# Kernel tuning notes

Measured on AMD Instinct MI355X. Metric: run time of the kernel, lower is better.

Reference implementation:

```python
import jax, jax.numpy as jnp
import numpy as np

N = 4096        # n_locations
D_MODEL = 512
H, D_K, D_V = 4, 128, 256


def setup_inputs() -> dict:
    key = jax.random.key(0)
    ks = jax.random.split(key, 7)
    s = 0.02
    return {
        "Q": jax.random.normal(ks[0], (N, D_MODEL), dtype=jnp.float32),
        "K": jax.random.normal(ks[1], (N, D_MODEL), dtype=jnp.float32),
        "V": jax.random.normal(ks[2], (N, D_MODEL), dtype=jnp.float32),
        "Wq": jax.random.normal(ks[3], (H, D_MODEL, D_K), dtype=jnp.float32) * s,
        "Wk": jax.random.normal(ks[4], (H, D_MODEL, D_K), dtype=jnp.float32) * s,
        "Wv": jax.random.normal(ks[5], (H, D_MODEL, D_V), dtype=jnp.float32) * s,
        "Wo": jax.random.normal(ks[6], (D_MODEL, H * D_V), dtype=jnp.float32) * s,
    }


def reference(Q, K, V, Wq, Wk, Wv, Wo):
    n = K.shape[0]
    # Batched per-head projections: [h, n, d_k] / [h, n, d_v]
    q = jnp.einsum('nd,hdk->hnk', Q, Wq)
    k = jnp.einsum('nd,hdk->hnk', K, Wk)
    v = jnp.einsum('nd,hdv->hnv', V, Wv)
    # NOTE: original scales by sqrt(n_locations) (K.size(0)), not sqrt(d_k)
    scores = jnp.einsum('hqk,hnk->hqn', q, k) / jnp.sqrt(jnp.asarray(n, q.dtype))
    weights = jax.nn.softmax(scores, axis=-1)          # [h, n, n]
    heads = jnp.einsum('hqn,hnv->hqv', weights, v)      # [h, n, d_v]
    # concat heads along feature dim: [n, h*d_v]
    x = jnp.transpose(heads, (1, 0, 2)).reshape(heads.shape[1], -1)
    return x @ Wo.T                                     # [n, d_model]
```

## Files before the change

### kernel.cpp

```cpp
#include <hip/hip_runtime.h>
#include <hip/hip_bf16.h>
#include <type_traits>

typedef __hip_bfloat16 bf16;
typedef __attribute__((ext_vector_type(8))) short bf16x8;
typedef __attribute__((ext_vector_type(4))) float f32x4;

#define N_LOC 4096

__device__ __forceinline__ bf16 to_bf16(float f) { return __float2bfloat16(f); }

__device__ __forceinline__ void dma16(const bf16* g, bf16* l) {
  __builtin_amdgcn_global_load_lds((const __attribute__((address_space(1))) unsigned int*)g,
                                   (__attribute__((address_space(3))) unsigned int*)l, 16, 0, 0);
}

__global__ __launch_bounds__(256) void prep(const float* __restrict__ Q, const float* __restrict__ K,
                                            const float* __restrict__ V, const float* __restrict__ Wo,
                                            bf16* __restrict__ Qb, bf16* __restrict__ Kb,
                                            bf16* __restrict__ Vb, bf16* __restrict__ Wob,
                                            const float* __restrict__ Wq, const float* __restrict__ Wk,
                                            const float* __restrict__ Wv,
                                            bf16* __restrict__ oq, bf16* __restrict__ ok,
                                            bf16* __restrict__ ov) {
  __shared__ float tile[64][65];
  if (blockIdx.x < 3328) {
    long i = ((long)blockIdx.x * 256 + threadIdx.x) * 8;
    const float* src;
    bf16* dst;
    long off;
    if (i < 2097152)      { src = Q;  dst = Qb;  off = i; }
    else if (i < 4194304) { src = K;  dst = Kb;  off = i - 2097152; }
    else if (i < 6291456) { src = V;  dst = Vb;  off = i - 4194304; }
    else                  { src = Wo; dst = Wob; off = i - 6291456; }
    float4 a = *(const float4*)&src[off];
    float4 b = *(const float4*)&src[off + 4];
    union { bf16 h[8]; bf16x8 v; } u;
    u.h[0] = to_bf16(a.x); u.h[1] = to_bf16(a.y); u.h[2] = to_bf16(a.z); u.h[3] = to_bf16(a.w);
    u.h[4] = to_bf16(b.x); u.h[5] = to_bf16(b.y); u.h[6] = to_bf16(b.z); u.h[7] = to_bf16(b.w);
    *(bf16x8*)&dst[off] = u.v;
  } else {
    int pid = blockIdx.x - 3328;
    int z = pid >> 7;
    int rem = pid & 127;
    int xx = rem & 7, y = rem >> 3;
    const float* W = (z == 0) ? Wq : (z == 1) ? Wk : Wv;
    bf16* out = (z == 0) ? oq : (z == 1) ? ok : ov;
    int DH = (z == 2) ? 256 : 128;
    int nt = DH >> 6;
    if (y >= 4 * nt) return;
    int h = y / nt, tt = y - h * nt;
    int d0 = xx * 64, t0 = tt * 64;
    for (int i = threadIdx.x; i < 4096; i += 256) {
      int r = i >> 6, c = i & 63;
      tile[r][c] = W[((size_t)h * 512 + d0 + r) * DH + t0 + c];
    }
    __syncthreads();
    for (int i = threadIdx.x; i < 4096; i += 256) {
      int t = i >> 6, d = i & 63;
      out[((size_t)(h * DH + t0 + t)) * 512 + d0 + d] = to_bf16(tile[d][t]);
    }
  }
}

template <int BN, int MODE, typename OutT>
__device__ __forceinline__ void gemm_body(const bf16* __restrict__ A, const bf16* __restrict__ Bt,
                                          OutT* __restrict__ C, int N, int K, int m0, int n0,
                                          bf16* sm) {
  constexpr int WN = BN / 2, JN = WN / 16, NB = BN / 32;
  int tid = threadIdx.x, lane = tid & 63, w = tid >> 6;
  int quad = lane >> 4, l16 = lane & 15;
  int wm = (w >> 1) * 64, wn = (w & 1) * WN;
  int srow = lane >> 3;
  int sG = (lane & 7) ^ srow;

  bf16* Asb[2] = { sm, sm + 8192 };
  bf16* Bsb[2] = { sm + 16384, sm + 16384 + BN * 64 };

  const bf16* ga[4];
  const bf16* gb[NB];
#pragma unroll
  for (int j = 0; j < 4; j++) ga[j] = A + (long)(m0 + (4 * j + w) * 8 + srow) * K + sG * 8;
#pragma unroll
  for (int j = 0; j < NB; j++) gb[j] = Bt + (long)(n0 + (4 * j + w) * 8 + srow) * K + sG * 8;

  auto stage = [&](int b) {
#pragma unroll
    for (int j = 0; j < 4; j++) { dma16(ga[j], &Asb[b][(4 * j + w) * 512]); ga[j] += 64; }
#pragma unroll
    for (int j = 0; j < NB; j++) { dma16(gb[j], &Bsb[b][(4 * j + w) * 512]); gb[j] += 64; }
  };

  f32x4 acc[4][JN] = {};
  stage(0);
  asm volatile("" ::: "memory");
  int cur = 0;
  const int NK = K >> 6;
  for (int s = 0; s < NK; ++s) {
    if (s + 1 < NK) {
      stage(cur ^ 1);
      if constexpr (NB == 4) asm volatile("s_waitcnt vmcnt(8)" ::: "memory");
      else                   asm volatile("s_waitcnt vmcnt(6)" ::: "memory");
    } else {
      asm volatile("s_waitcnt vmcnt(0)" ::: "memory");
    }
    __builtin_amdgcn_s_barrier();
    asm volatile("" ::: "memory");
    const bf16* Ac = Asb[cur];
    const bf16* Bc = Bsb[cur];
#pragma unroll
    for (int kk = 0; kk < 2; kk++) {
      bf16x8 af[4], bfr[JN];
#pragma unroll
      for (int i = 0; i < 4; i++) {
        int r = wm + i * 16 + l16;
        af[i] = *(const bf16x8*)&Ac[r * 64 + (((kk * 4 + quad) ^ r) & 7) * 8];
      }
#pragma unroll
      for (int j = 0; j < JN; j++) {
        int r = wn + j * 16 + l16;
        bfr[j] = *(const bf16x8*)&Bc[r * 64 + (((kk * 4 + quad) ^ r) & 7) * 8];
      }
#pragma unroll
      for (int i = 0; i < 4; i++)
#pragma unroll
        for (int j = 0; j < JN; j++)
          acc[i][j] = __builtin_amdgcn_mfma_f32_16x16x32_bf16(af[i], bfr[j], acc[i][j], 0, 0, 0);
    }
    asm volatile("" ::: "memory");
    __builtin_amdgcn_s_barrier();
    asm volatile("" ::: "memory");
    cur ^= 1;
  }

  if constexpr (MODE == 2) {
    bf16* tp = sm;
#pragma unroll
    for (int i = 0; i < 4; i++)
#pragma unroll
      for (int j = 0; j < JN; j++)
#pragma unroll
        for (int r = 0; r < 4; r++)
          tp[(wn + j * 16 + l16) * 136 + wm + i * 16 + quad * 4 + r] = to_bf16(acc[i][j][r]);
    __syncthreads();
#pragma unroll
    for (int it = 0; it < 8; ++it) {
      int idx = it * 256 + tid;
      int rown = idx >> 4, c8 = (idx & 15) * 8;
      *(bf16x8*)&C[(size_t)(n0 + rown) * 4096 + m0 + c8] = *(const bf16x8*)&tp[rown * 136 + c8];
    }
  } else {
#pragma unroll
    for (int i = 0; i < 4; i++)
#pragma unroll
      for (int j = 0; j < JN; j++)
#pragma unroll
        for (int r = 0; r < 4; r++) {
          long row = m0 + wm + i * 16 + quad * 4 + r;
          long col = n0 + wn + j * 16 + l16;
          if constexpr (MODE == 0)
            C[row * N + col] = to_bf16(acc[i][j][r]);
          else
            C[row * N + col] = acc[i][j][r];
        }
  }
}

__global__ __launch_bounds__(256) void proj_gemm(const bf16* __restrict__ QKVb,
                                                 const bf16* __restrict__ Wt,
                                                 bf16* __restrict__ qkout,
                                                 bf16* __restrict__ vTout) {
  __shared__ __align__(16) bf16 sm[4 * 128 * 64];
  int bid = blockIdx.x;
  if (bid < 256) {
    int z = bid >> 7;
    int t = bid & 127;
    int m0 = (t & 31) * 128, n0 = (t >> 5) * 128;
    gemm_body<128, 0, bf16>(QKVb + (size_t)z * 2097152, Wt + (size_t)z * 262144,
                            qkout + (size_t)z * 2097152, 512, 512, m0, n0, sm);
  } else {
    int t = bid - 256;
    int m0 = (t & 31) * 128, n0 = (t >> 5) * 128;
    gemm_body<128, 2, bf16>(QKVb + (size_t)2 * 2097152, Wt + (size_t)2 * 262144,
                            vTout, 1024, 512, m0, n0, sm);
  }
}

__global__ __launch_bounds__(256) void out_gemm(const bf16* __restrict__ xin,
                                                const bf16* __restrict__ Wob,
                                                float* __restrict__ outp) {
  __shared__ __align__(16) bf16 sm[2 * 128 * 64 + 2 * 64 * 64];
  gemm_body<64, 1, float>(xin, Wob, outp, 512, 1024, blockIdx.x * 128, blockIdx.y * 64, sm);
}

__global__ __launch_bounds__(512, 4) void attn(const bf16* __restrict__ qb,
                                               const bf16* __restrict__ kb,
                                               const bf16* __restrict__ vT,
                                               bf16* __restrict__ x) {
  __shared__ __align__(16) bf16 kt[2][64 * 128];
  __shared__ __align__(16) bf16 vt[2][128 * 64];
  __shared__ __align__(16) bf16 pt[64 * 72];
  __shared__ float Lrow[64];

  const int bid = blockIdx.x;
  const int xcd = bid & 7;
  const int head = xcd & 3;
  const int dvh = xcd >> 2;
  const int q0 = (bid >> 3) * 64;
  const int tid = threadIdx.x;
  const int lane = tid & 63, w = tid >> 6;
  const int quad = lane >> 4, l16 = lane & 15;
  const int cd = w & 3;
  const int g = w >> 2;

  bf16x8 onesf;
  {
    union { bf16 h[8]; bf16x8 v; } u;
    bf16 one = to_bf16(1.0f), zero = to_bf16(0.0f);
#pragma unroll
    for (int j = 0; j < 8; j++) u.h[j] = (l16 == 0) ? one : zero;
    onesf = u.v;
  }

  bf16x8 qf[2][4];
#pragma unroll
  for (int i = 0; i < 2; i++) {
    const bf16* qrow = &qb[(size_t)(q0 + g * 32 + i * 16 + l16) * 512 + head * 128];
#pragma unroll
    for (int kk = 0; kk < 4; kk++) qf[i][kk] = *(const bf16x8*)&qrow[kk * 32 + quad * 8];
  }

  f32x4 oacc[2][2] = {};
  f32x4 oL[2] = {};
  const float scale = 1.0f / 64.0f;

  const int j0 = 2 * w, j1 = 2 * w + 1;
  const bf16 *kp0, *kp1, *vp0, *vp1;
  {
    int r0 = 4 * j0 + (lane >> 4), r1 = 4 * j1 + (lane >> 4);
    int p = lane & 15;
    int G0 = (p & 8) | ((p ^ r0) & 7), G1 = (p & 8) | ((p ^ r1) & 7);
    kp0 = kb + (size_t)r0 * 512 + head * 128 + G0 * 8;
    kp1 = kb + (size_t)r1 * 512 + head * 128 + G1 * 8;
  }
  {
    int r0 = 8 * j0 + (lane >> 3), r1 = 8 * j1 + (lane >> 3);
    int p = lane & 7;
    int G0 = (p ^ r0) & 7, G1 = (p ^ r1) & 7;
    vp0 = vT + (size_t)(head * 256 + dvh * 128 + r0) * 4096 + G0 * 8;
    vp1 = vT + (size_t)(head * 256 + dvh * 128 + r1) * 4096 + G1 * 8;
  }

#define STAGE(b)                                        \
  do {                                                  \
    dma16(kp0, &kt[b][j0 * 512]);                       \
    dma16(kp1, &kt[b][j1 * 512]);                       \
    dma16(vp0, &vt[b][j0 * 512]);                       \
    dma16(vp1, &vt[b][j1 * 512]);                       \
    kp0 += 64 * 512; kp1 += 64 * 512;                   \
    vp0 += 64; vp1 += 64;                               \
  } while (0)

  STAGE(0);
  asm volatile("" ::: "memory");
  int cur = 0;

  for (int t = 0; t < 64; ++t) {
    if (t < 63) {
      STAGE(cur ^ 1);
      asm volatile("s_waitcnt vmcnt(4)" ::: "memory");
    } else {
      asm volatile("s_waitcnt vmcnt(0)" ::: "memory");
    }
    __builtin_amdgcn_s_barrier();
    asm volatile("" ::: "memory");

    const bf16* ktc = kt[cur];
    f32x4 sacc[2] = {};
#pragma unroll
    for (int kk = 0; kk < 4; kk++) {
      int R = cd * 16 + l16;
      int G = kk * 4 + quad;
      bf16x8 kf = *(const bf16x8*)&ktc[R * 128 + (((G ^ R) & 7) | (G & 8)) * 8];
      sacc[0] = __builtin_amdgcn_mfma_f32_16x16x32_bf16(qf[0][kk], kf, sacc[0], 0, 0, 0);
      sacc[1] = __builtin_amdgcn_mfma_f32_16x16x32_bf16(qf[1][kk], kf, sacc[1], 0, 0, 0);
    }
#pragma unroll
    for (int i = 0; i < 2; i++)
#pragma unroll
      for (int r = 0; r < 4; r++)
        pt[(g * 32 + i * 16 + quad * 4 + r) * 72 + cd * 16 + l16] =
            to_bf16(__expf(sacc[i][r] * scale));
    asm volatile("s_waitcnt lgkmcnt(0)" ::: "memory");
    __builtin_amdgcn_s_barrier();
    asm volatile("" ::: "memory");

    const bf16* vtc = vt[cur];
#pragma unroll
    for (int kk = 0; kk < 2; kk++) {
      bf16x8 pf[2];
#pragma unroll
      for (int i = 0; i < 2; i++)
        pf[i] = *(const bf16x8*)&pt[(g * 32 + i * 16 + l16) * 72 + kk * 32 + quad * 8];
#pragma unroll
      for (int c = 0; c < 2; c++) {
        int R = cd * 32 + c * 16 + l16;
        int G = kk * 4 + quad;
        bf16x8 vf = *(const bf16x8*)&vtc[R * 64 + ((G ^ R) & 7) * 8];
#pragma unroll
        for (int i = 0; i < 2; i++)
          oacc[i][c] = __builtin_amdgcn_mfma_f32_16x16x32_bf16(pf[i], vf, oacc[i][c], 0, 0, 0);
      }
      if (cd == 3) {
#pragma unroll
        for (int i = 0; i < 2; i++)
          oL[i] = __builtin_amdgcn_mfma_f32_16x16x32_bf16(pf[i], onesf, oL[i], 0, 0, 0);
      }
    }
    asm volatile("" ::: "memory");
    __builtin_amdgcn_s_barrier();
    asm volatile("" ::: "memory");
    cur ^= 1;
  }
#undef STAGE

  if (cd == 3 && l16 == 0) {
#pragma unroll
    for (int i = 0; i < 2; i++)
#pragma unroll
      for (int r = 0; r < 4; r++) Lrow[g * 32 + i * 16 + quad * 4 + r] = oL[i][r];
  }
  __syncthreads();

#pragma unroll
  for (int i = 0; i < 2; i++)
#pragma unroll
    for (int c = 0; c < 2; c++)
#pragma unroll
      for (int r = 0; r < 4; r++) {
        int row = g * 32 + i * 16 + quad * 4 + r;
        float v = oacc[i][c][r] / Lrow[row];
        x[(size_t)(q0 + row) * 1024 + head * 256 + dvh * 128 + cd * 32 + c * 16 + l16] =
            to_bf16(v);
      }
}

extern "C" void kernel_launch(void* const* d_in, const int* in_sizes, int n_in,
                              void* d_out, int out_size, void* d_ws, size_t ws_size,
                              hipStream_t stream) {
  const float* Q  = (const float*)d_in[0];
  const float* Km = (const float*)d_in[1];
  const float* V  = (const float*)d_in[2];
  const float* Wq = (const float*)d_in[3];
  const float* Wk = (const float*)d_in[4];
  const float* Wv = (const float*)d_in[5];
  const float* Wo = (const float*)d_in[6];
  float* out = (float*)d_out;

  bf16* ws  = (bf16*)d_ws;
  bf16* Qb  = ws;
  bf16* Kb  = Qb + 2097152;
  bf16* Vb  = Kb + 2097152;
  bf16* Wqt = Vb + 2097152;
  bf16* Wkt = Wqt + 262144;
  bf16* Wvt = Wkt + 262144;
  bf16* Wob = Wvt + 524288;
  bf16* qb  = Wob + 524288;
  bf16* kb  = qb + 2097152;
  bf16* vT  = kb + 2097152;
  bf16* x   = vT + 4194304;

  prep<<<3712, 256, 0, stream>>>(Q, Km, V, Wo, Qb, Kb, Vb, Wob, Wq, Wk, Wv, Wqt, Wkt, Wvt);

  proj_gemm<<<512, 256, 0, stream>>>(Qb, Wqt, qb, vT);

  attn<<<512, 512, 0, stream>>>(qb, kb, vT, x);

  out_gemm<<<dim3(32, 8), 256, 0, stream>>>(x, Wob, out);
}
```

Baseline: 214.2 us.

## Restructure attention so each wave owns 16 query rows, removing cross-wave barriers

The attention kernel goes from 8 waves per block, which split key columns and value columns and shared P through LDS, to 4 waves per block. Each wave now owns 16 query rows and computes the full 64-key score tile and all 128 value columns itself. Operands are swapped so P is stored transposed per wave, and the softmax denominator is a register sum plus shuffles instead of an MFMA against ones. This removes two block barriers per iteration and the Lrow LDS round-trip. In exchange, the next tile's prefetch is only issued after a full vmcnt(0) wait, so loads overlap less with compute, register pressure per wave rises, and there are fewer waves per block.

```diff
diff --git a/kernel.cpp b/kernel.cpp
--- a/kernel.cpp
+++ b/kernel.cpp
@@ -193,14 +193,13 @@
   gemm_body<64, 1, float>(xin, Wob, outp, 512, 1024, blockIdx.x * 128, blockIdx.y * 64, sm);
 }
 
-__global__ __launch_bounds__(512, 4) void attn(const bf16* __restrict__ qb,
+__global__ __launch_bounds__(256, 2) void attn(const bf16* __restrict__ qb,
                                                const bf16* __restrict__ kb,
                                                const bf16* __restrict__ vT,
                                                bf16* __restrict__ x) {
   __shared__ __align__(16) bf16 kt[2][64 * 128];
   __shared__ __align__(16) bf16 vt[2][128 * 64];
-  __shared__ __align__(16) bf16 pt[64 * 72];
-  __shared__ float Lrow[64];
+  __shared__ __align__(16) bf16 pt[4 * 16 * 72];
 
   const int bid = blockIdx.x;
   const int xcd = bid & 7;
@@ -210,139 +209,111 @@
   const int tid = threadIdx.x;
   const int lane = tid & 63, w = tid >> 6;
   const int quad = lane >> 4, l16 = lane & 15;
-  const int cd = w & 3;
-  const int g = w >> 2;
-
-  bf16x8 onesf;
+  const int qw = q0 + w * 16;
+  bf16* ptw = &pt[w * 16 * 72];
+
+  bf16x8 qfB[4];
   {
-    union { bf16 h[8]; bf16x8 v; } u;
-    bf16 one = to_bf16(1.0f), zero = to_bf16(0.0f);
-#pragma unroll
-    for (int j = 0; j < 8; j++) u.h[j] = (l16 == 0) ? one : zero;
-    onesf = u.v;
-  }
-
-  bf16x8 qf[2][4];
-#pragma unroll
-  for (int i = 0; i < 2; i++) {
-    const bf16* qrow = &qb[(size_t)(q0 + g * 32 + i * 16 + l16) * 512 + head * 128];
-#pragma unroll
-    for (int kk = 0; kk < 4; kk++) qf[i][kk] = *(const bf16x8*)&qrow[kk * 32 + quad * 8];
-  }
-
-  f32x4 oacc[2][2] = {};
-  f32x4 oL[2] = {};
+    const bf16* qrow = &qb[(size_t)(qw + l16) * 512 + head * 128];
+#pragma unroll
+    for (int kk = 0; kk < 4; kk++) qfB[kk] = *(const bf16x8*)&qrow[kk * 32 + quad * 8];
+  }
+
+  f32x4 oacc[8] = {};
+  float Lp = 0.0f;
   const float scale = 1.0f / 64.0f;
 
-  const int j0 = 2 * w, j1 = 2 * w + 1;
-  const bf16 *kp0, *kp1, *vp0, *vp1;
-  {
-    int r0 = 4 * j0 + (lane >> 4), r1 = 4 * j1 + (lane >> 4);
-    int p = lane & 15;
-    int G0 = (p & 8) | ((p ^ r0) & 7), G1 = (p & 8) | ((p ^ r1) & 7);
-    kp0 = kb + (size_t)r0 * 512 + head * 128 + G0 * 8;
-    kp1 = kb + (size_t)r1 * 512 + head * 128 + G1 * 8;
-  }
-  {
-    int r0 = 8 * j0 + (lane >> 3), r1 = 8 * j1 + (lane >> 3);
-    int p = lane & 7;
-    int G0 = (p ^ r0) & 7, G1 = (p ^ r1) & 7;
-    vp0 = vT + (size_t)(head * 256 + dvh * 128 + r0) * 4096 + G0 * 8;
-    vp1 = vT + (size_t)(head * 256 + dvh * 128 + r1) * 4096 + G1 * 8;
-  }
-
-#define STAGE(b)                                        \
-  do {                                                  \
-    dma16(kp0, &kt[b][j0 * 512]);                       \
-    dma16(kp1, &kt[b][j1 * 512]);                       \
-    dma16(vp0, &vt[b][j0 * 512]);                       \
-    dma16(vp1, &vt[b][j1 * 512]);                       \
-    kp0 += 64 * 512; kp1 += 64 * 512;                   \
-    vp0 += 64; vp1 += 64;                               \
-  } while (0)
+  const bf16* kpa[4];
+  const bf16* vpa[4];
+#pragma unroll
+  for (int t2 = 0; t2 < 4; t2++) {
+    int j = 4 * w + t2;
+    {
+      int r = 4 * j + (lane >> 4);
+      int p = lane & 15;
+      int G = (p & 8) | ((p ^ r) & 7);
+      kpa[t2] = kb + (size_t)r * 512 + head * 128 + G * 8;
+    }
+    {
+      int r = 8 * j + (lane >> 3);
+      int p = lane & 7;
+      int G = (p ^ r) & 7;
+      vpa[t2] = vT + (size_t)(head * 256 + dvh * 128 + r) * 4096 + G * 8;
+    }
+  }
+  auto STAGE = [&](int b) {
+#pragma unroll
+    for (int t2 = 0; t2 < 4; t2++) {
+      dma16(kpa[t2], &kt[b][(4 * w + t2) * 512]); kpa[t2] += 64 * 512;
+      dma16(vpa[t2], &vt[b][(4 * w + t2) * 512]); vpa[t2] += 64;
+    }
+  };
 
   STAGE(0);
   asm volatile("" ::: "memory");
   int cur = 0;
 
   for (int t = 0; t < 64; ++t) {
-    if (t < 63) {
-      STAGE(cur ^ 1);
-      asm volatile("s_waitcnt vmcnt(4)" ::: "memory");
-    } else {
-      asm volatile("s_waitcnt vmcnt(0)" ::: "memory");
-    }
+    asm volatile("s_waitcnt vmcnt(0)" ::: "memory");
     __builtin_amdgcn_s_barrier();
     asm volatile("" ::: "memory");
+    if (t < 63) STAGE(cur ^ 1);
 
     const bf16* ktc = kt[cur];
-    f32x4 sacc[2] = {};
-#pragma unroll
-    for (int kk = 0; kk < 4; kk++) {
-      int R = cd * 16 + l16;
-      int G = kk * 4 + quad;
-      bf16x8 kf = *(const bf16x8*)&ktc[R * 128 + (((G ^ R) & 7) | (G & 8)) * 8];
-      sacc[0] = __builtin_amdgcn_mfma_f32_16x16x32_bf16(qf[0][kk], kf, sacc[0], 0, 0, 0);
-      sacc[1] = __builtin_amdgcn_mfma_f32_16x16x32_bf16(qf[1][kk], kf, sacc[1], 0, 0, 0);
-    }
-#pragma unroll
-    for (int i = 0; i < 2; i++)
-#pragma unroll
-      for (int r = 0; r < 4; r++)
-        pt[(g * 32 + i * 16 + quad * 4 + r) * 72 + cd * 16 + l16] =
-            to_bf16(__expf(sacc[i][r] * scale));
-    asm volatile("s_waitcnt lgkmcnt(0)" ::: "memory");
-    __builtin_amdgcn_s_barrier();
-    asm volatile("" ::: "memory");
+    f32x4 sacc[4] = {};
+#pragma unroll
+    for (int kb4 = 0; kb4 < 4; kb4++) {
+      int R = kb4 * 16 + l16;
+#pragma unroll
+      for (int kk = 0; kk < 4; kk++) {
+        int G = kk * 4 + quad;
+        bf16x8 kf = *(const bf16x8*)&ktc[R * 128 + (((G ^ R) & 7) | (G & 8)) * 8];
+        sacc[kb4] = __builtin_amdgcn_mfma_f32_16x16x32_bf16(kf, qfB[kk], sacc[kb4], 0, 0, 0);
+      }
+    }
+
+#pragma unroll
+    for (int kb4 = 0; kb4 < 4; kb4++) {
+      float p0 = __expf(sacc[kb4][0] * scale);
+      float p1 = __expf(sacc[kb4][1] * scale);
+      float p2 = __expf(sacc[kb4][2] * scale);
+      float p3 = __expf(sacc[kb4][3] * scale);
+      Lp += (p0 + p1) + (p2 + p3);
+      union { bf16 h[4]; uint2 u; } pk;
+      pk.h[0] = to_bf16(p0); pk.h[1] = to_bf16(p1);
+      pk.h[2] = to_bf16(p2); pk.h[3] = to_bf16(p3);
+      *(uint2*)&ptw[l16 * 72 + kb4 * 16 + quad * 4] = pk.u;
+    }
 
     const bf16* vtc = vt[cur];
 #pragma unroll
     for (int kk = 0; kk < 2; kk++) {
-      bf16x8 pf[2];
-#pragma unroll
-      for (int i = 0; i < 2; i++)
-        pf[i] = *(const bf16x8*)&pt[(g * 32 + i * 16 + l16) * 72 + kk * 32 + quad * 8];
-#pragma unroll
-      for (int c = 0; c < 2; c++) {
-        int R = cd * 32 + c * 16 + l16;
+      bf16x8 pf = *(const bf16x8*)&ptw[l16 * 72 + kk * 32 + quad * 8];
+#pragma unroll
+      for (int c = 0; c < 8; c++) {
+        int R = c * 16 + l16;
         int G = kk * 4 + quad;
         bf16x8 vf = *(const bf16x8*)&vtc[R * 64 + ((G ^ R) & 7) * 8];
-#pragma unroll
-        for (int i = 0; i < 2; i++)
-          oacc[i][c] = __builtin_amdgcn_mfma_f32_16x16x32_bf16(pf[i], vf, oacc[i][c], 0, 0, 0);
+        oacc[c] = __builtin_amdgcn_mfma_f32_16x16x32_bf16(vf, pf, oacc[c], 0, 0, 0);
       }
-      if (cd == 3) {
-#pragma unroll
-        for (int i = 0; i < 2; i++)
-          oL[i] = __builtin_amdgcn_mfma_f32_16x16x32_bf16(pf[i], onesf, oL[i], 0, 0, 0);
-      }
-    }
-    asm volatile("" ::: "memory");
-    __builtin_amdgcn_s_barrier();
-    asm volatile("" ::: "memory");
+    }
     cur ^= 1;
   }
-#undef STAGE
-
-  if (cd == 3 && l16 == 0) {
-#pragma unroll
-    for (int i = 0; i < 2; i++)
-#pragma unroll
-      for (int r = 0; r < 4; r++) Lrow[g * 32 + i * 16 + quad * 4 + r] = oL[i][r];
-  }
-  __syncthreads();
-
-#pragma unroll
-  for (int i = 0; i < 2; i++)
-#pragma unroll
-    for (int c = 0; c < 2; c++)
-#pragma unroll
-      for (int r = 0; r < 4; r++) {
-        int row = g * 32 + i * 16 + quad * 4 + r;
-        float v = oacc[i][c][r] / Lrow[row];
-        x[(size_t)(q0 + row) * 1024 + head * 256 + dvh * 128 + cd * 32 + c * 16 + l16] =
-            to_bf16(v);
-      }
+
+  float Lf = Lp;
+  Lf += __shfl_xor(Lf, 16);
+  Lf += __shfl_xor(Lf, 32);
+  float inv = 1.0f / Lf;
+
+#pragma unroll
+  for (int c = 0; c < 8; c++) {
+    union { bf16 h[4]; uint2 u; } ok;
+    ok.h[0] = to_bf16(oacc[c][0] * inv);
+    ok.h[1] = to_bf16(oacc[c][1] * inv);
+    ok.h[2] = to_bf16(oacc[c][2] * inv);
+    ok.h[3] = to_bf16(oacc[c][3] * inv);
+    *(uint2*)&x[(size_t)(qw + l16) * 1024 + head * 256 + dvh * 128 + c * 16 + quad * 4] = ok.u;
+  }
 }
 
 extern "C" void kernel_launch(void* const* d_in, const int* in_sizes, int n_in,
@@ -374,7 +345,7 @@
 
   proj_gemm<<<512, 256, 0, stream>>>(Qb, Wqt, qb, vT);
 
-  attn<<<512, 512, 0, stream>>>(qb, kb, vT, x);
+  attn<<<512, 256, 0, stream>>>(qb, kb, vT, x);
 
   out_gemm<<<dim3(32, 8), 256, 0, stream>>>(x, Wob, out);
 }
```

Measured after the change: 224.7 us. +4.9%, slower.

## Software-pipeline attention loop so QK^T of next tile overlaps PV of current

Applied to the files above, without the earlier changes.

Restructures the flash-attention inner loop into a skewed pipeline. The score MFMAs and exp for tile t+1 are issued in the same phase as the P·V MFMAs for tile t, and K and V loads are staged separately with adjusted vmcnt waits. P fragments are read into registers before a barrier so the pt buffer can be overwritten in the same iteration. This removes one barrier per iteration and gives the scheduler independent MFMA and exp work to interleave. In exchange it raises register pressure and makes the buffer-indexing and wait logic more fragile.

```diff
diff --git a/kernel.cpp b/kernel.cpp
--- a/kernel.cpp
+++ b/kernel.cpp
@@ -251,78 +251,129 @@
     vp1 = vT + (size_t)(head * 256 + dvh * 128 + r1) * 4096 + G1 * 8;
   }
 
-#define STAGE(b)                                        \
+#define STAGE_K(b)                                      \
   do {                                                  \
     dma16(kp0, &kt[b][j0 * 512]);                       \
     dma16(kp1, &kt[b][j1 * 512]);                       \
+    kp0 += 64 * 512; kp1 += 64 * 512;                   \
+  } while (0)
+#define STAGE_V(b)                                      \
+  do {                                                  \
     dma16(vp0, &vt[b][j0 * 512]);                       \
     dma16(vp1, &vt[b][j1 * 512]);                       \
-    kp0 += 64 * 512; kp1 += 64 * 512;                   \
     vp0 += 64; vp1 += 64;                               \
   } while (0)
 
-  STAGE(0);
+#define S_PHASE(buf)                                                            \
+  do {                                                                          \
+    const bf16* ktc = kt[buf];                                                  \
+    f32x4 sacc[2] = {};                                                         \
+    _Pragma("unroll")                                                           \
+    for (int kk = 0; kk < 4; kk++) {                                            \
+      int R = cd * 16 + l16;                                                    \
+      int G = kk * 4 + quad;                                                    \
+      bf16x8 kf = *(const bf16x8*)&ktc[R * 128 + (((G ^ R) & 7) | (G & 8)) * 8];\
+      sacc[0] = __builtin_amdgcn_mfma_f32_16x16x32_bf16(qf[0][kk], kf, sacc[0], 0, 0, 0); \
+      sacc[1] = __builtin_amdgcn_mfma_f32_16x16x32_bf16(qf[1][kk], kf, sacc[1], 0, 0, 0); \
+    }                                                                           \
+    _Pragma("unroll")                                                           \
+    for (int i = 0; i < 2; i++)                                                 \
+      _Pragma("unroll")                                                         \
+      for (int r = 0; r < 4; r++)                                               \
+        pt[(g * 32 + i * 16 + quad * 4 + r) * 72 + cd * 16 + l16] =             \
+            to_bf16(__expf(sacc[i][r] * scale));                                \
+  } while (0)
+
+  STAGE_K(0);
+  STAGE_V(0);
+  STAGE_K(1);
+  asm volatile("s_waitcnt vmcnt(2)" ::: "memory");
+  __builtin_amdgcn_s_barrier();
   asm volatile("" ::: "memory");
-  int cur = 0;
+  S_PHASE(0);
+  asm volatile("s_waitcnt lgkmcnt(0)" ::: "memory");
+  __builtin_amdgcn_s_barrier();
+  asm volatile("" ::: "memory");
 
   for (int t = 0; t < 64; ++t) {
-    if (t < 63) {
-      STAGE(cur ^ 1);
-      asm volatile("s_waitcnt vmcnt(4)" ::: "memory");
-    } else {
-      asm volatile("s_waitcnt vmcnt(0)" ::: "memory");
-    }
-    __builtin_amdgcn_s_barrier();
-    asm volatile("" ::: "memory");
-
-    const bf16* ktc = kt[cur];
-    f32x4 sacc[2] = {};
-#pragma unroll
-    for (int kk = 0; kk < 4; kk++) {
-      int R = cd * 16 + l16;
-      int G = kk * 4 + quad;
-      bf16x8 kf = *(const bf16x8*)&ktc[R * 128 + (((G ^ R) & 7) | (G & 8)) * 8];
-      sacc[0] = __builtin_amdgcn_mfma_f32_16x16x32_bf16(qf[0][kk], kf, sacc[0], 0, 0, 0);
-      sacc[1] = __builtin_amdgcn_mfma_f32_16x16x32_bf16(qf[1][kk], kf, sacc[1], 0, 0, 0);
-    }
-#pragma unroll
-    for (int i = 0; i < 2; i++)
-#pragma unroll
-      for (int r = 0; r < 4; r++)
-        pt[(g * 32 + i * 16 + quad * 4 + r) * 72 + cd * 16 + l16] =
-            to_bf16(__expf(sacc[i][r] * scale));
+    bf16x8 pf[2][2];
+#pragma unroll
+    for (int kk = 0; kk < 2; kk++)
+#pragma unroll
+      for (int i = 0; i < 2; i++)
+        pf[kk][i] = *(const bf16x8*)&pt[(g * 32 + i * 16 + l16) * 72 + kk * 32 + quad * 8];
     asm volatile("s_waitcnt lgkmcnt(0)" ::: "memory");
     __builtin_amdgcn_s_barrier();
     asm volatile("" ::: "memory");
 
-    const bf16* vtc = vt[cur];
-#pragma unroll
-    for (int kk = 0; kk < 2; kk++) {
-      bf16x8 pf[2];
+    if (t < 62) STAGE_K(t & 1);
+    if (t < 63) STAGE_V((t + 1) & 1);
+    if (t < 62)      asm volatile("s_waitcnt vmcnt(4)" ::: "memory");
+    else if (t == 62) asm volatile("s_waitcnt vmcnt(2)" ::: "memory");
+    else              asm volatile("s_waitcnt vmcnt(0)" ::: "memory");
+
+    if (t < 63) {
+      const bf16* ktc = kt[(t + 1) & 1];
+      f32x4 sacc[2] = {};
+#pragma unroll
+      for (int kk = 0; kk < 4; kk++) {
+        int R = cd * 16 + l16;
+        int G = kk * 4 + quad;
+        bf16x8 kf = *(const bf16x8*)&ktc[R * 128 + (((G ^ R) & 7) | (G & 8)) * 8];
+        sacc[0] = __builtin_amdgcn_mfma_f32_16x16x32_bf16(qf[0][kk], kf, sacc[0], 0, 0, 0);
+        sacc[1] = __builtin_amdgcn_mfma_f32_16x16x32_bf16(qf[1][kk], kf, sacc[1], 0, 0, 0);
+      }
+      const bf16* vtc = vt[t & 1];
+#pragma unroll
+      for (int kk = 0; kk < 2; kk++) {
+#pragma unroll
+        for (int c = 0; c < 2; c++) {
+          int R = cd * 32 + c * 16 + l16;
+          int G = kk * 4 + quad;
+          bf16x8 vf = *(const bf16x8*)&vtc[R * 64 + ((G ^ R) & 7) * 8];
+#pragma unroll
+          for (int i = 0; i < 2; i++)
+            oacc[i][c] = __builtin_amdgcn_mfma_f32_16x16x32_bf16(pf[kk][i], vf, oacc[i][c], 0, 0, 0);
+        }
+        if (cd == 3) {
+#pragma unroll
+          for (int i = 0; i < 2; i++)
+            oL[i] = __builtin_amdgcn_mfma_f32_16x16x32_bf16(pf[kk][i], onesf, oL[i], 0, 0, 0);
+        }
+      }
 #pragma unroll
       for (int i = 0; i < 2; i++)
-        pf[i] = *(const bf16x8*)&pt[(g * 32 + i * 16 + l16) * 72 + kk * 32 + quad * 8];
-#pragma unroll
-      for (int c = 0; c < 2; c++) {
-        int R = cd * 32 + c * 16 + l16;
-        int G = kk * 4 + quad;
-        bf16x8 vf = *(const bf16x8*)&vtc[R * 64 + ((G ^ R) & 7) * 8];
-#pragma unroll
-        for (int i = 0; i < 2; i++)
-          oacc[i][c] = __builtin_amdgcn_mfma_f32_16x16x32_bf16(pf[i], vf, oacc[i][c], 0, 0, 0);
-      }
-      if (cd == 3) {
-#pragma unroll
-        for (int i = 0; i < 2; i++)
-          oL[i] = __builtin_amdgcn_mfma_f32_16x16x32_bf16(pf[i], onesf, oL[i], 0, 0, 0);
-      }
-    }
-    asm volatile("" ::: "memory");
+#pragma unroll
+        for (int r = 0; r < 4; r++)
+          pt[(g * 32 + i * 16 + quad * 4 + r) * 72 + cd * 16 + l16] =
+              to_bf16(__expf(sacc[i][r] * scale));
+    } else {
+      const bf16* vtc = vt[t & 1];
+#pragma unroll
+      for (int kk = 0; kk < 2; kk++) {
+#pragma unroll
+        for (int c = 0; c < 2; c++) {
+          int R = cd * 32 + c * 16 + l16;
+          int G = kk * 4 + quad;
+          bf16x8 vf = *(const bf16x8*)&vtc[R * 64 + ((G ^ R) & 7) * 8];
+#pragma unroll
+          for (int i = 0; i < 2; i++)
+            oacc[i][c] = __builtin_amdgcn_mfma_f32_16x16x32_bf16(pf[kk][i], vf, oacc[i][c], 0, 0, 0);
+        }
+        if (cd == 3) {
+#pragma unroll
+          for (int i = 0; i < 2; i++)
+            oL[i] = __builtin_amdgcn_mfma_f32_16x16x32_bf16(pf[kk][i], onesf, oL[i], 0, 0, 0);
+        }
+      }
+    }
+    asm volatile("s_waitcnt lgkmcnt(0)" ::: "memory");
     __builtin_amdgcn_s_barrier();
     asm volatile("" ::: "memory");
-    cur ^= 1;
-  }
-#undef STAGE
+  }
+#undef STAGE_K
+#undef STAGE_V
+#undef S_PHASE
 
   if (cd == 3 && l16 == 0) {
 #pragma unroll
```

Result: no change. 211.0 us (-1.5%).
